# Kernel optimization log

Measured on AMD Instinct MI355X. Metric: run time of the kernel, lower is better.

Reference implementation:

```python
import jax, jax.numpy as jnp
import numpy as np

N, E, C = 50000, 10000, 500
NNZ = 400000
IN_DIM, EDGE_DIM, NODE_DIM, COMP_DIM = 128, 128, 128, 128


def _glorot(key, shape):
    fan = shape[0] + shape[1]
    return jax.random.normal(key, shape, jnp.float32) * (2.0 / fan) ** 0.5


def _seg_mean(vals, idx, num):
    # mean aggregation over segments (scatter-add + count normalize)
    s = jax.ops.segment_sum(vals, idx, num_segments=num)
    cnt = jax.ops.segment_sum(jnp.ones((idx.shape[0], 1), vals.dtype), idx, num_segments=num)
    return s / jnp.maximum(cnt, 1.0)


def _prelu(v, a):
    return jnp.where(v >= 0, v, a * v)


def _conv(x, ni, ei, ec_e, ec_c, nc_n, nc_c, n_nodes, n_edges, n_comps,
          Wne, Wen, Wec, Wnc, a):
    # node -> hyperedge message passing
    e = _seg_mean((x @ Wne)[ni], ei, n_edges)            # [E, edge_dim]
    e_act = _prelu(e, a)
    # hyperedge -> node
    n = _seg_mean((e_act @ Wen)[ei], ni, n_nodes)        # [N, node_dim]
    # edge -> component and node -> component
    c = _seg_mean((e_act @ Wec)[ec_e], ec_c, n_comps) + \
        _seg_mean((x @ Wnc)[nc_n], nc_c, n_comps)        # [C, comp_dim]
    return n, e, c


def setup_inputs() -> dict:
    key = jax.random.key(0)
    ks = jax.random.split(key, 16)
    x = jax.random.normal(ks[0], (N, IN_DIM), jnp.float32)
    hyperedge_index = jnp.stack([
        jax.random.randint(ks[1], (NNZ,), 0, N),
        jax.random.randint(ks[2], (NNZ,), 0, E),
    ])
    hyperedge_component_index = jnp.stack([
        jnp.arange(E), jax.random.randint(ks[3], (E,), 0, C)])
    node_component_index = jnp.stack([
        jnp.arange(N), jax.random.randint(ks[4], (N,), 0, C)])
    return dict(
        x=x,
        hyperedge_index=hyperedge_index,
        hyperedge_component_index=hyperedge_component_index,
        node_component_index=node_component_index,
        num_nodes=N, num_edges=E, num_components=C,
        W_ne0=_glorot(ks[5], (IN_DIM, EDGE_DIM)),
        W_en0=_glorot(ks[6], (EDGE_DIM, NODE_DIM)),
        W_ec0=_glorot(ks[7], (EDGE_DIM, COMP_DIM)),
        W_nc0=_glorot(ks[8], (IN_DIM, COMP_DIM)),
        W_ne1=_glorot(ks[9], (NODE_DIM, EDGE_DIM)),
        W_en1=_glorot(ks[10], (EDGE_DIM, NODE_DIM)),
        W_ec1=_glorot(ks[11], (EDGE_DIM, COMP_DIM)),
        W_nc1=_glorot(ks[12], (NODE_DIM, COMP_DIM)),
        prelu_a=jnp.array(0.25, jnp.float32),
    )


def reference(x, hyperedge_index, hyperedge_component_index, node_component_index,
              num_nodes, num_edges, num_components,
              W_ne0, W_en0, W_ec0, W_nc0, W_ne1, W_en1, W_ec1, W_nc1, prelu_a):
    ni, ei = hyperedge_index[0], hyperedge_index[1]
    ec_e, ec_c = hyperedge_component_index[0], hyperedge_component_index[1]
    nc_n, nc_c = node_component_index[0], node_component_index[1]
    layers = [(W_ne0, W_en0, W_ec0, W_nc0), (W_ne1, W_en1, W_ec1, W_nc1)]
    e_out = c_out = None
    for Wne, Wen, Wec, Wnc in layers:
        n_out, e_out, c_out = _conv(x, ni, ei, ec_e, ec_c, nc_n, nc_c,
                                    num_nodes, num_edges, num_components,
                                    Wne, Wen, Wec, Wnc, prelu_a)
        x = _prelu(n_out, prelu_a)  # HyperEncoder applies act between/after layers
    return (x, e_out, c_out)
```

## Files before the change

### kernel.cpp

```cpp
#include <hip/hip_runtime.h>
#include <stdint.h>

typedef unsigned int u32;
typedef _Float16 f16;
typedef f16 half8 __attribute__((ext_vector_type(8)));
typedef float f32x4 __attribute__((ext_vector_type(4)));
#define TS 4096
#define KB2 256
#define CH 2048

__device__ __forceinline__ float bflo(u32 u) { return __uint_as_float(u << 16); }
__device__ __forceinline__ float bfhi(u32 u) { return __uint_as_float(u & 0xffff0000u); }
__device__ __forceinline__ u32 f2bf(float x) {
    u32 u = __float_as_uint(x);
    return (u + 0x7fffu + ((u >> 16) & 1u)) >> 16;
}
__device__ __forceinline__ u32 pack2(float a, float b) { return f2bf(a) | (f2bf(b) << 16); }

__device__ __forceinline__ int bstart2(int b, int total) {
    return (int)(((unsigned long long)b * (u32)total + KB2 - 1) / KB2);
}

__device__ __forceinline__ int blk_exscan(int v, int& total) {
    __shared__ int ws[5];
    int t = threadIdx.x, lane = t & 63, w = t >> 6;
    int inc = v;
    for (int d = 1; d < 64; d <<= 1) { int u = __shfl_up(inc, d, 64); if (lane >= d) inc += u; }
    __syncthreads();
    if (lane == 63) ws[w] = inc;
    __syncthreads();
    if (t == 0) { int acc = 0; for (int i = 0; i < 4; ++i) { int x = ws[i]; ws[i] = acc; acc += x; } ws[4] = acc; }
    __syncthreads();
    total = ws[4];
    return ws[w] + (inc - v);
}

#define ACC8(v) do { \
    a[0] += bflo((v).x); a[1] += bfhi((v).x); a[2] += bflo((v).y); a[3] += bfhi((v).y); \
    a[4] += bflo((v).z); a[5] += bfhi((v).z); a[6] += bflo((v).w); a[7] += bfhi((v).w); } while (0)

__device__ __forceinline__ void seg_mean8(const u32* __restrict__ in,
                                          const int* __restrict__ items,
                                          const int* __restrict__ off,
                                          int nseg, int nrows, int seg, float a[8]) {
    int lane = threadIdx.x & 63;
    int rs = lane >> 4;
    int cc = lane & 15;
#pragma unroll
    for (int i = 0; i < 8; ++i) a[i] = 0.f;
    int s0 = 0, s1 = 0;
    if (seg < nseg) { s0 = off[seg]; s1 = off[seg + 1]; }
    const uint4* rows = (const uint4*)in;
    int base = s0;
    for (; base + 16 <= s1; base += 16) {
        u32 r0 = (u32)items[base + rs];
        u32 r1 = (u32)items[base + 4 + rs];
        u32 r2 = (u32)items[base + 8 + rs];
        u32 r3 = (u32)items[base + 12 + rs];
        r0 = (r0 < (u32)nrows) ? r0 : 0u;
        r1 = (r1 < (u32)nrows) ? r1 : 0u;
        r2 = (r2 < (u32)nrows) ? r2 : 0u;
        r3 = (r3 < (u32)nrows) ? r3 : 0u;
        uint4 v0 = rows[(size_t)r0 * 16 + cc];
        uint4 v1 = rows[(size_t)r1 * 16 + cc];
        uint4 v2 = rows[(size_t)r2 * 16 + cc];
        uint4 v3 = rows[(size_t)r3 * 16 + cc];
        ACC8(v0); ACC8(v1); ACC8(v2); ACC8(v3);
    }
    for (; base + 8 <= s1; base += 8) {
        u32 r0 = (u32)items[base + rs];
        u32 r1 = (u32)items[base + 4 + rs];
        r0 = (r0 < (u32)nrows) ? r0 : 0u;
        r1 = (r1 < (u32)nrows) ? r1 : 0u;
        uint4 v0 = rows[(size_t)r0 * 16 + cc];
        uint4 v1 = rows[(size_t)r1 * 16 + cc];
        ACC8(v0); ACC8(v1);
    }
    int idx = base + rs;
    if (idx < s1) {
        u32 r = (u32)items[idx]; r = (r < (u32)nrows) ? r : 0u;
        uint4 v = rows[(size_t)r * 16 + cc];
        ACC8(v);
    }
    idx += 4;
    if (idx < s1) {
        u32 r = (u32)items[idx]; r = (r < (u32)nrows) ? r : 0u;
        uint4 v = rows[(size_t)r * 16 + cc];
        ACC8(v);
    }
#pragma unroll
    for (int i = 0; i < 8; ++i) {
        a[i] += __shfl_xor(a[i], 16, 64);
        a[i] += __shfl_xor(a[i], 32, 64);
    }
    float inv = 1.f / fmaxf((float)(s1 - s0), 1.f);
#pragma unroll
    for (int i = 0; i < 8; ++i) a[i] *= inv;
}

__device__ __forceinline__ void agg4_body(const u32* __restrict__ in,
                                          const int* __restrict__ items,
                                          const int* __restrict__ off,
                                          float* __restrict__ out_f32,
                                          u32* __restrict__ out_bf,
                                          int nseg, int nrows, int do_prelu,
                                          const float* __restrict__ alpha_p, int seg,
                                          int nt) {
    if (seg >= nseg) return;
    int lane = threadIdx.x & 63;
    int rs = lane >> 4;
    int cc = lane & 15;
    float a[8];
    seg_mean8(in, items, off, nseg, nrows, seg, a);
    if (do_prelu) {
        float al = *alpha_p;
#pragma unroll
        for (int i = 0; i < 8; ++i) a[i] = (a[i] >= 0.f) ? a[i] : al * a[i];
    }
    if (rs == 0) {
        if (out_f32) {
            float* o = out_f32 + ((size_t)seg << 7) + cc * 8;
            f32x4 v0 = {a[0], a[1], a[2], a[3]};
            f32x4 v1 = {a[4], a[5], a[6], a[7]};
            if (nt) {
                __builtin_nontemporal_store(v0, (f32x4*)o);
                __builtin_nontemporal_store(v1, (f32x4*)(o + 4));
            } else {
                *(f32x4*)o = v0;
                *(f32x4*)(o + 4) = v1;
            }
        }
        if (out_bf) {
            uint4 pk;
            pk.x = pack2(a[0], a[1]); pk.y = pack2(a[2], a[3]);
            pk.z = pack2(a[4], a[5]); pk.w = pack2(a[6], a[7]);
            *(uint4*)(out_bf + ((size_t)seg << 6) + cc * 4) = pk;
        }
    }
}

__device__ __forceinline__ void aggh_body(const u32* __restrict__ in,
                                          const int* __restrict__ items,
                                          const int* __restrict__ off,
                                          f16* __restrict__ outh,
                                          int nseg, int nrows, int seg) {
    if (seg >= nseg) return;
    float a[8];
    seg_mean8(in, items, off, nseg, nrows, seg, a);
    int lane = threadIdx.x & 63, rs = lane >> 4, cc = lane & 15;
    if (rs == 0) {
        union { f16 h[8]; uint4 v; } u;
#pragma unroll
        for (int i = 0; i < 8; ++i) u.h[i] = (f16)a[i];
        *(uint4*)(outh + ((size_t)seg << 7) + cc * 8) = u.v;
    }
}

__device__ __forceinline__ void gemm1_body(const float* __restrict__ A,
                                           const f16* __restrict__ WL,
                                           float* __restrict__ out, int M,
                                           int rb, int accum, int nt) {
    int t = threadIdx.x, lane = t & 63, wv = t >> 6;
    int r0 = (wv >> 1) << 4, ctb = (wv & 1) << 2;
    int frow = lane & 15, fk = (lane >> 4) << 3;
    int rl0 = r0 + ((lane >> 4) << 2);
    int ar = rb + r0 + frow;
    f32x4 acc[4];
#pragma unroll
    for (int j = 0; j < 4; ++j) {
        int c = ((ctb + j) << 4) + frow;
#pragma unroll
        for (int rg = 0; rg < 4; ++rg) {
            int row = rb + rl0 + rg;
            acc[j][rg] = (accum && row < M) ? out[((size_t)row << 7) + c] : 0.f;
        }
    }
#pragma unroll
    for (int ks = 0; ks < 4; ++ks) {
        int kb = ks * 32 + fk;
        half8 af;
        if (ar < M) {
            float4 a0 = *(const float4*)(A + ((size_t)ar << 7) + kb);
            float4 a1 = *(const float4*)(A + ((size_t)ar << 7) + kb + 4);
            af[0] = (f16)a0.x; af[1] = (f16)a0.y; af[2] = (f16)a0.z; af[3] = (f16)a0.w;
            af[4] = (f16)a1.x; af[5] = (f16)a1.y; af[6] = (f16)a1.z; af[7] = (f16)a1.w;
        } else {
#pragma unroll
            for (int j = 0; j < 8; ++j) af[j] = (f16)0.f;
        }
#pragma unroll
        for (int j = 0; j < 4; ++j) {
            int c = ((ctb + j) << 4) + frow;
            half8 bf = *(const half8*)(WL + ((size_t)c << 7) + kb);
            acc[j] = __builtin_amdgcn_mfma_f32_16x16x32_f16(af, bf, acc[j], 0, 0, 0);
        }
    }
#pragma unroll
    for (int j = 0; j < 4; ++j) {
        int c = ((ctb + j) << 4) + frow;
#pragma unroll
        for (int rg = 0; rg < 4; ++rg) {
            int row = rb + rl0 + rg;
            if (row < M) {
                if (nt) __builtin_nontemporal_store(acc[j][rg], out + ((size_t)row << 7) + c);
                else out[((size_t)row << 7) + c] = acc[j][rg];
            }
        }
    }
}

__global__ __launch_bounds__(256) void k_front(
        const int* __restrict__ ni, const int* __restrict__ ei,
        const int* __restrict__ nc_c, const int* __restrict__ ec_c,
        int* __restrict__ bcntE, int* __restrict__ bcntN,
        int* __restrict__ cnt_cn, int* __restrict__ cnt_ce,
        int nnz, int n, int e, int nbh,
        int* __restrict__ ticket,
        int* __restrict__ basesE, int* __restrict__ basesN,
        int* __restrict__ bcur_e, int* __restrict__ bcur_n,
        int* __restrict__ off_cn, int* __restrict__ off_ce,
        int* __restrict__ cur_cn, int* __restrict__ cur_ce, int c,
        const float* __restrict__ W0, const float* __restrict__ W1,
        const float* __restrict__ W2, const float* __restrict__ W3,
        const float* __restrict__ W4, const float* __restrict__ W5,
        f16* __restrict__ wt6) {
    int t = threadIdx.x;
    int b = blockIdx.x;
    if (b >= nbh) {
        int gid = (b - nbh) * 256 + t;
        if (gid >= 8 * 2048) return;
        int m = gid >> 11;
        int rem = gid & 2047;
        int cq = rem >> 4;
        int s = rem & 15;
        const float* W = (m == 0) ? W0 : (m == 1) ? W1 : (m == 2) ? W2 :
                         (m == 3) ? W3 : (m == 4) ? W4 : (m == 5) ? W5 :
                         (m == 6) ? W4 : W5;
        int khi = (m < 6) ? (((s & 7) ^ (cq & 7)) | (s & 8)) : s;
        int k0 = khi << 3;
        union { f16 h[8]; uint4 v; } u;
#pragma unroll
        for (int j = 0; j < 8; ++j) u.h[j] = (f16)W[((k0 + j) << 7) + cq];
        *(uint4*)(wt6 + ((size_t)m << 14) + (cq << 7) + (s << 3)) = u.v;
        return;
    }
    __shared__ int hE[KB2], hN[KB2];
    __shared__ int lastflag;
    hE[t] = 0; hN[t] = 0;
    __syncthreads();
    int base = b * CH;
    int lim = base + CH; if (lim > nnz) lim = nnz;
    for (int i = base + t; i < lim; i += 256) {
        u32 v = (u32)ni[i], eg = (u32)ei[i];
        if (v >= (u32)n) v = 0;
        if (eg >= (u32)e) eg = 0;
        atomicAdd(&hE[(int)(((unsigned long long)eg * KB2) / (u32)e)], 1);
        atomicAdd(&hN[(int)(((unsigned long long)v  * KB2) / (u32)n)], 1);
    }
    __syncthreads();
    if (hE[t]) atomicAdd(&bcntE[t], hE[t]);
    if (hN[t]) atomicAdd(&bcntN[t], hN[t]);
    int gid = b * 256 + t, stride = nbh * 256;
    for (int j = gid; j < n + e; j += stride) {
        if (j < n) atomicAdd(&cnt_cn[nc_c[j]], 1);
        else       atomicAdd(&cnt_ce[ec_c[j - n]], 1);
    }
    __syncthreads();
    if (t == 0) {
        __threadfence();
        lastflag = (atomicAdd(ticket, 1) == nbh - 1);
    }
    __syncthreads();
    if (!lastflag) return;
    __threadfence();
    int tot;
    int v = bcntE[t];
    int ex = blk_exscan(v, tot);
    basesE[t] = ex; bcur_e[t] = ex;
    if (t == 0) basesE[KB2] = tot;
    v = bcntN[t];
    ex = blk_exscan(v, tot);
    basesN[t] = ex; bcur_n[t] = ex;
    if (t == 0) basesN[KB2] = tot;
    int i0 = 2 * t, i1 = 2 * t + 1;
    int v0 = (i0 < c) ? cnt_cn[i0] : 0;
    int v1 = (i1 < c) ? cnt_cn[i1] : 0;
    ex = blk_exscan(v0 + v1, tot);
    if (i0 < c) { off_cn[i0] = ex;      cur_cn[i0] = ex; }
    if (i1 < c) { off_cn[i1] = ex + v0; cur_cn[i1] = ex + v0; }
    if (t == 0) off_cn[c] = tot;
    v0 = (i0 < c) ? cnt_ce[i0] : 0;
    v1 = (i1 < c) ? cnt_ce[i1] : 0;
    ex = blk_exscan(v0 + v1, tot);
    if (i0 < c) { off_ce[i0] = ex;      cur_ce[i0] = ex; }
    if (i1 < c) { off_ce[i1] = ex + v0; cur_ce[i1] = ex + v0; }
    if (t == 0) off_ce[c] = tot;
}

__global__ __launch_bounds__(256) void k_part_a(
        const int* __restrict__ ni, const int* __restrict__ ei,
        int* __restrict__ bcur_e, int* __restrict__ bcur_n,
        u32* __restrict__ stg_e, u32* __restrict__ stg_n,
        const int* __restrict__ nc_n, const int* __restrict__ nc_c,
        const int* __restrict__ ec_e, const int* __restrict__ ec_c,
        int* __restrict__ cur_cn, int* __restrict__ cur_ce,
        int* __restrict__ csr_cn, int* __restrict__ csr_ce,
        const float2* __restrict__ xin, u32* __restrict__ xout, int npairs,
        int nnz, int n, int e, int nbh) {
    __shared__ u32 pk[CH];
    __shared__ unsigned short bb[CH];
    __shared__ int hist[KB2];
    __shared__ int gb[KB2];
    int t = threadIdx.x;
    int bx = blockIdx.x;
    if (bx >= 2 * nbh) {
        int j = (bx - 2 * nbh) * 256 + t;
        if (j < npairs) { float2 v = xin[j]; xout[j] = pack2(v.x, v.y); }
        return;
    }
    int side = bx >= nbh;
    int pb = side ? bx - nbh : bx;
    int base = pb * CH;
    int cnt  = nnz - base; if (cnt > CH) cnt = CH;
    for (int i = t; i < KB2; i += 256) hist[i] = 0;
    __syncthreads();
    u32 total = side ? (u32)n : (u32)e;
    for (int i = t; i < cnt; i += 256) {
        int v = ni[base + i], eg = ei[base + i];
        u32 key = side ? (u32)v : (u32)eg;
        u32 pay = side ? (u32)eg : (u32)v;
        if (key >= total) key = 0;
        u32 b = (u32)(((unsigned long long)key * KB2) / total);
        pk[i] = side ? (pay | (key << 14)) : (pay | (key << 16));
        bb[i] = (unsigned short)b;
        atomicAdd(&hist[b], 1);
    }
    __syncthreads();
    int* cursor = side ? bcur_n : bcur_e;
    u32* stg    = side ? stg_n  : stg_e;
    if (t < KB2) {
        int h = hist[t];
        gb[t] = h ? atomicAdd(&cursor[t], h) : 0;
        hist[t] = 0;
    }
    __syncthreads();
    for (int i = t; i < cnt; i += 256) {
        int b = bb[i];
        int r = atomicAdd(&hist[b], 1);
        stg[gb[b] + r] = pk[i];
    }
    int gid = pb * 256 + t;
    int stride = nbh * 256;
    if (side == 0) {
        for (int j = gid; j < e; j += stride) { int c = ec_c[j]; csr_ce[atomicAdd(&cur_ce[c], 1)] = ec_e[j]; }
    } else {
        for (int j = gid; j < n; j += stride) { int c = nc_c[j]; csr_cn[atomicAdd(&cur_cn[c], 1)] = nc_n[j]; }
    }
}

__global__ __launch_bounds__(256) void k_part_b2(
        const u32* __restrict__ stg_e, const u32* __restrict__ stg_n,
        const int* __restrict__ basesE, const int* __restrict__ basesN,
        int* __restrict__ off_e, int* __restrict__ off_n,
        int* __restrict__ csr_e, int* __restrict__ csr_n, int e, int n) {
    __shared__ int lcnt[256];
    int b = blockIdx.x, t = threadIdx.x;
    const u32* stg; const int* bases; int* off; int* csr; int total; int shift; u32 mask;
    if (b < KB2) { stg = stg_e; bases = basesE; off = off_e; csr = csr_e; total = e; shift = 16; mask = 0xFFFFu; }
    else { b -= KB2; stg = stg_n; bases = basesN; off = off_n; csr = csr_n; total = n; shift = 14; mask = 0x3FFFu; }
    int lo = bstart2(b, total), hi = bstart2(b + 1, total);
    int nid = hi - lo;
    int sbase = bases[b], send = bases[b + 1];
    lcnt[t] = 0;
    __syncthreads();
    for (int i = sbase + t; i < send; i += 256) {
        int key = (int)(stg[i] >> shift);
        atomicAdd(&lcnt[key - lo], 1);
    }
    __syncthreads();
    int cval = (t < nid) ? lcnt[t] : 0;
    int tot;
    int ex = blk_exscan(cval, tot);
    int cursor = sbase + ex;
    if (t < nid) { off[lo + t] = cursor; lcnt[t] = cursor; }
    if (t == 0 && hi == total) off[total] = send;
    __syncthreads();
    for (int i = sbase + t; i < send; i += 256) {
        u32 s = stg[i];
        int key = (int)(s >> shift);
        int pay = (int)(s & mask);
        int p = atomicAdd(&lcnt[key - lo], 1);
        csr[p] = pay;
    }
}

__global__ void k_cvt(const float2* __restrict__ in, u32* __restrict__ out, int npairs) {
    int j = blockIdx.x * blockDim.x + threadIdx.x;
    if (j < npairs) { float2 v = in[j]; out[j] = pack2(v.x, v.y); }
}

__global__ void k_hist_fb(const int* __restrict__ ni, const int* __restrict__ ei,
                          const int* __restrict__ nc_c, const int* __restrict__ ec_c,
                          int* __restrict__ deg_e, int* __restrict__ deg_n,
                          int* __restrict__ cnt_cn, int* __restrict__ cnt_ce,
                          int nnz, int n, int e) {
    int j = blockIdx.x * blockDim.x + threadIdx.x;
    if (j < nnz) {
        atomicAdd(&deg_e[ei[j]], 1);
        atomicAdd(&deg_n[ni[j]], 1);
    }
    if (j < n) atomicAdd(&cnt_cn[nc_c[j]], 1);
    if (j < e) atomicAdd(&cnt_ce[ec_c[j]], 1);
}

__device__ __forceinline__ void scan_sel(int b, int t0, int t01, int t012,
        const int* c0, int* o0, int* u0, int n0,
        const int* c1, int* o1, int* u1, int n1,
        const int* c2, int* o2, int* u2, int n2,
        const int* c3, int* o3, int* u3, int n3,
        const int*& cnt, int*& off, int*& cur, int& n, int& tile) {
    if (b < t0)        { cnt = c0; off = o0; cur = u0; n = n0; tile = b; }
    else if (b < t01)  { cnt = c1; off = o1; cur = u1; n = n1; tile = b - t0; }
    else if (b < t012) { cnt = c2; off = o2; cur = u2; n = n2; tile = b - t01; }
    else               { cnt = c3; off = o3; cur = u3; n = n3; tile = b - t012; }
}

__global__ void k_scan_p1(const int* c0, int n0, const int* c1, int n1,
                          const int* c2, int n2, const int* c3, int n3,
                          int t0, int t01, int t012, int* __restrict__ tilesum) {
    __shared__ int ws[4];
    int b = blockIdx.x;
    const int* cnt; int* off; int* cur; int n; int tile;
    scan_sel(b, t0, t01, t012, c0, nullptr, nullptr, n0, c1, nullptr, nullptr, n1,
             c2, nullptr, nullptr, n2, c3, nullptr, nullptr, n3, cnt, off, cur, n, tile);
    int base = tile * TS + threadIdx.x * 16;
    int s = 0;
#pragma unroll
    for (int i = 0; i < 16; ++i) { int idx = base + i; if (idx < n) s += cnt[idx]; }
    for (int d = 32; d; d >>= 1) s += __shfl_xor(s, d, 64);
    int lane = threadIdx.x & 63, w = threadIdx.x >> 6;
    if (lane == 0) ws[w] = s;
    __syncthreads();
    if (threadIdx.x == 0) tilesum[b] = ws[0] + ws[1] + ws[2] + ws[3];
}

__global__ void k_scan_p2(const int* __restrict__ tilesum, int* __restrict__ tilebase,
                          int t0, int t01, int t012, int t0123,
                          int* o0, int n0, int* o1, int n1, int* o2, int n2, int* o3, int n3) {
    if (threadIdx.x != 0 || blockIdx.x != 0) return;
    int carry = 0;
    for (int b = 0;    b < t0;    ++b) { tilebase[b] = carry; carry += tilesum[b]; } o0[n0] = carry;
    carry = 0;
    for (int b = t0;   b < t01;   ++b) { tilebase[b] = carry; carry += tilesum[b]; } o1[n1] = carry;
    carry = 0;
    for (int b = t01;  b < t012;  ++b) { tilebase[b] = carry; carry += tilesum[b]; } o2[n2] = carry;
    carry = 0;
    for (int b = t012; b < t0123; ++b) { tilebase[b] = carry; carry += tilesum[b]; } o3[n3] = carry;
}

__global__ void k_scan_p3(const int* c0, int* o0, int* u0, int n0,
                          const int* c1, int* o1, int* u1, int n1,
                          const int* c2, int* o2, int* u2, int n2,
                          const int* c3, int* o3, int* u3, int n3,
                          int t0, int t01, int t012, const int* __restrict__ tilebase) {
    __shared__ int wsum[4];
    int b = blockIdx.x;
    const int* cnt; int* off; int* cur; int n; int tile;
    scan_sel(b, t0, t01, t012, c0, o0, u0, n0, c1, o1, u1, n1,
             c2, o2, u2, n2, c3, o3, u3, n3, cnt, off, cur, n, tile);
    int lane = threadIdx.x & 63, w = threadIdx.x >> 6;
    int base = tile * TS + threadIdx.x * 16;
    int vals[16];
    int s = 0;
#pragma unroll
    for (int i = 0; i < 16; ++i) { int idx = base + i; int v = (idx < n) ? cnt[idx] : 0; vals[i] = v; s += v; }
    int inc = s;
    for (int d = 1; d < 64; d <<= 1) { int u = __shfl_up(inc, d, 64); if (lane >= d) inc += u; }
    if (lane == 63) wsum[w] = inc;
    __syncthreads();
    if (threadIdx.x == 0) {
        int acc = tilebase[b];
        for (int i = 0; i < 4; ++i) { int t = wsum[i]; wsum[i] = acc; acc += t; }
    }
    __syncthreads();
    int ex = wsum[w] + (inc - s);
#pragma unroll
    for (int i = 0; i < 16; ++i) {
        int idx = base + i;
        if (idx < n) { off[idx] = ex; cur[idx] = ex; }
        ex += vals[i];
    }
}

__global__ void k_scatter(const int* __restrict__ ni, const int* __restrict__ ei,
                          const int* __restrict__ nc_n, const int* __restrict__ nc_c,
                          const int* __restrict__ ec_e, const int* __restrict__ ec_c,
                          int* __restrict__ cur_e, int* __restrict__ cur_n,
                          int* __restrict__ cur_cn, int* __restrict__ cur_ce,
                          int* __restrict__ csr_e, int* __restrict__ csr_n,
                          int* __restrict__ csr_cn, int* __restrict__ csr_ce,
                          int nnz, int n, int e) {
    int j = blockIdx.x * blockDim.x + threadIdx.x;
    if (j < nnz) {
        int v = ni[j], eg = ei[j];
        csr_e[atomicAdd(&cur_e[eg], 1)] = v;
        csr_n[atomicAdd(&cur_n[v], 1)] = eg;
    }
    if (j < n) { int c = nc_c[j]; csr_cn[atomicAdd(&cur_cn[c], 1)] = nc_n[j]; }
    if (j < e) { int c = ec_c[j]; csr_ce[atomicAdd(&cur_ce[c], 1)] = ec_e[j]; }
}

__global__ __launch_bounds__(256) void k_agg4(
        const u32* __restrict__ in, const int* __restrict__ items,
        const int* __restrict__ off, float* __restrict__ out_f32,
        u32* __restrict__ out_bf,
        int nseg, int nrows, int do_prelu, const float* __restrict__ alpha_p) {
    int seg = blockIdx.x * (blockDim.x >> 6) + (threadIdx.x >> 6);
    agg4_body(in, items, off, out_f32, out_bf, nseg, nrows, do_prelu, alpha_p, seg, 0);
}

__global__ __launch_bounds__(256) void k_agg4h(
        const u32* __restrict__ in, const int* __restrict__ items,
        const int* __restrict__ off, f16* __restrict__ outh,
        int nseg, int nrows) {
    int seg = blockIdx.x * (blockDim.x >> 6) + (threadIdx.x >> 6);
    aggh_body(in, items, off, outh, nseg, nrows, seg);
}

__global__ __launch_bounds__(256) void k_agg_final(
        const u32* __restrict__ ybf, const int* __restrict__ csr_n, const int* __restrict__ off_n,
        float* __restrict__ out_x, int n, int e,
        const u32* __restrict__ eactbf, const int* __restrict__ csr_ce, const int* __restrict__ off_ce,
        float* __restrict__ ca_e,
        const float* __restrict__ ca_n, const f16* __restrict__ WncL,
        float* __restrict__ out_c,
        int c, int nblkN, int ncb, const float* __restrict__ alpha_p) {
    int b = blockIdx.x;
    int wv = threadIdx.x >> 6;
    if (b < nblkN) {
        agg4_body(ybf, csr_n, off_n, out_x, nullptr, n, e, 1, alpha_p, b * 4 + wv, 1);
    } else if (b < nblkN + ncb) {
        agg4_body(eactbf, csr_ce, off_ce, ca_e, nullptr, c, e, 0, nullptr, (b - nblkN) * 4 + wv, 0);
    } else {
        gemm1_body(ca_n, WncL, out_c, c, (b - nblkN - ncb) * 32, 0, 0);
    }
}

__global__ __launch_bounds__(256) void k_gemm1(
        const float* __restrict__ A, const f16* __restrict__ WL,
        float* __restrict__ out, int M) {
    gemm1_body(A, WL, out, M, blockIdx.x * 32, 1, 1);
}

__global__ __launch_bounds__(256) void k_mlp_mfma(
        const f16* __restrict__ Ah,
        const f16* __restrict__ W1t, const f16* __restrict__ W2t,
        float* __restrict__ out_raw, u32* __restrict__ out_actbf,
        u32* __restrict__ out_ybf, int M, const float* __restrict__ alpha_p,
        int nmlp,
        const u32* __restrict__ cn_in, const int* __restrict__ cn_items,
        const int* __restrict__ cn_off, float* __restrict__ cn_out,
        int cn_nseg, int cn_nrows) {
    __shared__ f16 As[32 * 128];
    __shared__ f16 Wt[128 * 128];
    int t = threadIdx.x;
    if (blockIdx.x >= nmlp) {
        if (cn_out == nullptr) return;
        int seg = (blockIdx.x - nmlp) * 4 + (t >> 6);
        agg4_body(cn_in, cn_items, cn_off, cn_out, nullptr, cn_nseg, cn_nrows, 0,
                  alpha_p, seg, 0);
        return;
    }
    int rb = blockIdx.x * 32;
    float al = *alpha_p;
    {
        const uint4* src = (const uint4*)W1t;
        uint4* dst = (uint4*)Wt;
        for (int i = t; i < 2048; i += 256) dst[i] = src[i];
    }
    {
        const uint4* Ag = (const uint4*)Ah;
        for (int i = t; i < 512; i += 256) {
            int r = i >> 4, s = i & 15;
            int row = rb + r;
            uint4 v = make_uint4(0u, 0u, 0u, 0u);
            if (row < M) v = Ag[(size_t)row * 16 + s];
            *(uint4*)((char*)As + (r << 8) + ((s << 4) ^ ((r & 7) << 4))) = v;
        }
    }
    __syncthreads();

    int lane = t & 63, wv = t >> 6;
    int r0  = (wv >> 1) << 4;
    int ctb = (wv & 1) << 2;
    int frow = lane & 15;
    int fk = (lane >> 4) << 3;
    int rl0 = r0 + ((lane >> 4) << 2);
    int ar = r0 + frow;
    int asw = (ar & 7) << 4;

    f32x4 acc[4] = {{0.f,0.f,0.f,0.f},{0.f,0.f,0.f,0.f},{0.f,0.f,0.f,0.f},{0.f,0.f,0.f,0.f}};
#pragma unroll
    for (int ks = 0; ks < 4; ++ks) {
        int kb2 = (ks * 32 + fk) << 1;
        half8 a = *(const half8*)((const char*)As + (ar << 8) + (kb2 ^ asw));
#pragma unroll
        for (int j = 0; j < 4; ++j) {
            int c = ((ctb + j) << 4) + frow;
            half8 b = *(const half8*)((const char*)Wt + (c << 8) + (kb2 ^ ((c & 7) << 4)));
            acc[j] = __builtin_amdgcn_mfma_f32_16x16x32_f16(a, b, acc[j], 0, 0, 0);
        }
    }
    __syncthreads();
    {
        const uint4* src = (const uint4*)W2t;
        uint4* dst = (uint4*)Wt;
        for (int i = t; i < 2048; i += 256) dst[i] = src[i];
    }
#pragma unroll
    for (int j = 0; j < 4; ++j) {
        int c = ((ctb + j) << 4) + frow;
#pragma unroll
        for (int rg = 0; rg < 4; ++rg) {
            int rl = rl0 + rg;
            int row = rb + rl;
            float ev = acc[j][rg];
            if (out_raw != nullptr && row < M)
                __builtin_nontemporal_store(ev, out_raw + ((size_t)row << 7) + c);
            float av = (ev >= 0.f) ? ev : al * ev;
            float po = __shfl_xor(av, 1, 64);
            if (out_actbf != nullptr && (frow & 1) == 0 && row < M)
                out_actbf[((size_t)row << 6) + (c >> 1)] = pack2(av, po);
            *(f16*)((char*)As + (rl << 8) + (((c << 1)) ^ ((rl & 7) << 4))) = (f16)av;
        }
    }
    __syncthreads();
    f32x4 acc2[4] = {{0.f,0.f,0.f,0.f},{0.f,0.f,0.f,0.f},{0.f,0.f,0.f,0.f},{0.f,0.f,0.f,0.f}};
#pragma unroll
    for (int ks = 0; ks < 4; ++ks) {
        int kb2 = (ks * 32 + fk) << 1;
        half8 a = *(const half8*)((const char*)As + (ar << 8) + (kb2 ^ asw));
#pragma unroll
        for (int j = 0; j < 4; ++j) {
            int c = ((ctb + j) << 4) + frow;
            half8 b = *(const half8*)((const char*)Wt + (c << 8) + (kb2 ^ ((c & 7) << 4)));
            acc2[j] = __builtin_amdgcn_mfma_f32_16x16x32_f16(a, b, acc2[j], 0, 0, 0);
        }
    }
#pragma unroll
    for (int j = 0; j < 4; ++j) {
        int c = ((ctb + j) << 4) + frow;
#pragma unroll
        for (int rg = 0; rg < 4; ++rg) {
            int rl = rl0 + rg;
            int row = rb + rl;
            float yv = acc2[j][rg];
            float po = __shfl_xor(yv, 1, 64);
            if ((frow & 1) == 0 && row < M)
                out_ybf[((size_t)row << 6) + (c >> 1)] = pack2(yv, po);
        }
    }
}

extern "C" void kernel_launch(void* const* d_in, const int* in_sizes, int n_in,
                              void* d_out, int out_size, void* d_ws, size_t ws_size,
                              hipStream_t stream) {
    const int N   = in_sizes[0] / 128;
    const int NNZ = in_sizes[1] / 2;
    const int E   = in_sizes[2] / 2;
    const int C   = 500;

    const float* x0 = (const float*)d_in[0];
    const int* ni   = (const int*)d_in[1];
    const int* ei   = ni + NNZ;
    const int* ec_e = (const int*)d_in[2];
    const int* ec_c = ec_e + E;
    const int* nc_n = (const int*)d_in[3];
    const int* nc_c = nc_n + N;
    const float* Wne0 = (const float*)d_in[7];
    const float* Wen0 = (const float*)d_in[8];
    const float* Wne1 = (const float*)d_in[11];
    const float* Wen1 = (const float*)d_in[12];
    const float* Wec1 = (const float*)d_in[13];
    const float* Wnc1 = (const float*)d_in[14];
    const float* alpha = (const float*)d_in[15];

    float* out_x = (float*)d_out;
    float* out_e = out_x + (size_t)N * 128;
    float* out_c = out_e + (size_t)E * 128;

    char* w = (char*)d_ws;
    auto alloc = [&](size_t bytes) { char* p = w; w += (bytes + 255) & ~(size_t)255; return p; };
    int* zgrp   = (int*)alloc((size_t)(2 * KB2 + 2 * C + 1) * 4);
    int* bcntE  = zgrp;
    int* bcntN  = zgrp + KB2;
    int* cnt_cn = zgrp + 2 * KB2;
    int* cnt_ce = zgrp + 2 * KB2 + C;
    int* ticket = zgrp + 2 * KB2 + 2 * C;
    int* off_e  = (int*)alloc((size_t)(E + 1) * 4);
    int* off_n  = (int*)alloc((size_t)(N + 1) * 4);
    int* off_cn = (int*)alloc((size_t)(C + 1) * 4);
    int* off_ce = (int*)alloc((size_t)(C + 1) * 4);
    int* cur_cn = (int*)alloc((size_t)C * 4);
    int* cur_ce = (int*)alloc((size_t)C * 4);
    int* csr_e  = (int*)alloc((size_t)NNZ * 4);
    int* csr_n  = (int*)alloc((size_t)NNZ * 4);
    int* csr_cn = (int*)alloc((size_t)N * 4);
    int* csr_ce = (int*)alloc((size_t)E * 4);
    int* basesE = (int*)alloc((size_t)(KB2 + 1) * 4);
    int* basesN = (int*)alloc((size_t)(KB2 + 1) * 4);
    int* bcur_e = (int*)alloc(KB2 * 4);
    int* bcur_n = (int*)alloc(KB2 * 4);
    u32* stg_e  = (u32*)alloc((size_t)NNZ * 4);
    u32* stg_n  = (u32*)alloc((size_t)NNZ * 4);
    u32* xbf    = (u32*)alloc((size_t)N * 64 * 4);
    u32* x1bf   = (u32*)alloc((size_t)N * 64 * 4);
    u32* ybf    = (u32*)alloc((size_t)E * 64 * 4);
    u32* eactbf = (u32*)alloc((size_t)E * 64 * 4);
    f16* xah    = (f16*)alloc((size_t)E * 128 * 2);
    float* ca_e = (float*)alloc((size_t)C * 128 * 4);
    float* ca_n = (float*)alloc((size_t)C * 128 * 4);
    f16* wt6    = (f16*)alloc((size_t)8 * 16384 * 2);
    int* deg_e    = (int*)alloc((size_t)E * 4);
    int* deg_n    = (int*)alloc((size_t)N * 4);
    int* cur_e    = (int*)alloc((size_t)E * 4);
    int* cur_n    = (int*)alloc((size_t)N * 4);
    int* tilesum  = (int*)alloc(64 * 4);
    int* tilebase = (int*)alloc(64 * 4);

    const int th = 256;
    const int npairs = N * 64;
    const int nbh = (NNZ + CH - 1) / CH;
    const int nkc = (npairs + th - 1) / th;

    bool binned = (E <= 16384) && (N <= 65536) && (E >= KB2) && (N >= KB2) &&
                  ((N + KB2 - 1) / KB2 <= 256) && (C <= 512);
    const int nbh_eff = binned ? nbh : 0;

    hipMemsetAsync(zgrp, 0, (size_t)(2 * KB2 + 2 * C + 1) * 4, stream);
    k_front<<<nbh_eff + 64, 256, 0, stream>>>(
        ni, ei, nc_c, ec_c,
        bcntE, bcntN, cnt_cn, cnt_ce, NNZ, N, E, nbh_eff,
        ticket, basesE, basesN, bcur_e, bcur_n,
        off_cn, off_ce, cur_cn, cur_ce, C,
        Wne0, Wen0, Wne1, Wen1, Wec1, Wnc1, wt6);

    if (binned) {
        k_part_a<<<2 * nbh + nkc, 256, 0, stream>>>(
            ni, ei, bcur_e, bcur_n, stg_e, stg_n,
            nc_n, nc_c, ec_e, ec_c,
            cur_cn, cur_ce, csr_cn, csr_ce,
            (const float2*)x0, xbf, npairs, NNZ, N, E, nbh);
        k_part_b2<<<2 * KB2, 256, 0, stream>>>(stg_e, stg_n, basesE, basesN,
                                               off_e, off_n, csr_e, csr_n, E, N);
    } else {
        hipMemsetAsync(deg_e, 0, (size_t)E * 4, stream);
        hipMemsetAsync(deg_n, 0, (size_t)N * 4, stream);
        k_cvt<<<(npairs + th - 1) / th, th, 0, stream>>>((const float2*)x0, xbf, npairs);
        k_hist_fb<<<(NNZ > N + E ? NNZ : N + E) / th + 1, th, 0, stream>>>(
            ni, ei, nc_c, ec_c, deg_e, deg_n, cnt_cn, cnt_ce, NNZ, N, E);
        const int t0 = (E + TS - 1) / TS, t1 = (N + TS - 1) / TS;
        const int t2 = (C + TS - 1) / TS, t3 = (C + TS - 1) / TS;
        const int t01 = t0 + t1, t012 = t01 + t2, t0123 = t012 + t3;
        k_scan_p1<<<t0123, 256, 0, stream>>>(deg_e, E, deg_n, N, cnt_cn, C, cnt_ce, C,
                                             t0, t01, t012, tilesum);
        k_scan_p2<<<1, 64, 0, stream>>>(tilesum, tilebase, t0, t01, t012, t0123,
                                        off_e, E, off_n, N, off_cn, C, off_ce, C);
        k_scan_p3<<<t0123, 256, 0, stream>>>(deg_e, off_e, cur_e, E,
                                             deg_n, off_n, cur_n, N,
                                             cnt_cn, off_cn, cur_cn, C,
                                             cnt_ce, off_ce, cur_ce, C,
                                             t0, t01, t012, tilebase);
        k_scatter<<<(NNZ + th - 1) / th, th, 0, stream>>>(ni, ei, nc_n, nc_c, ec_e, ec_c,
                                                          cur_e, cur_n, cur_cn, cur_ce,
                                                          csr_e, csr_n, csr_cn, csr_ce, NNZ, N, E);
    }

    const int gmlp = (E + 31) / 32;
    const int ncb  = (C + 3) / 4;
    const int gc   = (C + 31) / 32;
    k_agg4h<<<(E + 3) / 4, 256, 0, stream>>>(xbf, csr_e, off_e, xah, E, N);
    k_mlp_mfma<<<gmlp, 256, 0, stream>>>(xah, wt6, wt6 + 16384, nullptr, nullptr, ybf,
                                         E, alpha, gmlp,
                                         nullptr, nullptr, nullptr, nullptr, 0, 0);
    k_agg4<<<(N + 3) / 4, 256, 0, stream>>>(ybf, csr_n, off_n, nullptr, x1bf, N, E, 1, alpha);
    k_agg4h<<<(E + 3) / 4, 256, 0, stream>>>(x1bf, csr_e, off_e, xah, E, N);
    k_mlp_mfma<<<gmlp + ncb, 256, 0, stream>>>(xah, wt6 + 2 * 16384, wt6 + 3 * 16384,
                                               out_e, eactbf, ybf, E, alpha, gmlp,
                                               x1bf, csr_cn, off_cn, ca_n, C, N);
    {
        const int nblkN = (N + 3) / 4;
        k_agg_final<<<nblkN + ncb + gc, 256, 0, stream>>>(
            ybf, csr_n, off_n, out_x, N, E,
            eactbf, csr_ce, off_ce, ca_e,
            ca_n, wt6 + 7 * 16384, out_c,
            C, nblkN, ncb, alpha);
    }
    k_gemm1<<<gc, 256, 0, stream>>>(ca_e, wt6 + 6 * 16384, out_c, C);
}
```

Before: 256.7 us.

## Vectorize CSR index loads in segment mean and merge binning passes

The segment-mean gather now loads neighbor indices as 16-byte and 8-byte vectors, and adds a 32-item unrolled loop so more row loads are in flight per lane. It also changes which item each lane accumulates, which is fine because summation order is free. The partition kernel now bins each nnz chunk for both the edge and node sides in a single block. This halves the grid and reads the ni/ei arrays once instead of twice. The tradeoffs are doubled shared memory per block and lower block-level parallelism in the partition step.

```diff
diff --git a/kernel.cpp b/kernel.cpp
--- a/kernel.cpp
+++ b/kernel.cpp
@@ -5,6 +5,8 @@
 typedef _Float16 f16;
 typedef f16 half8 __attribute__((ext_vector_type(8)));
 typedef float f32x4 __attribute__((ext_vector_type(4)));
+typedef uint4 uint4u __attribute__((aligned(4)));
+typedef uint2 uint2u __attribute__((aligned(4)));
 #define TS 4096
 #define KB2 256
 #define CH 2048
@@ -52,15 +54,31 @@
     if (seg < nseg) { s0 = off[seg]; s1 = off[seg + 1]; }
     const uint4* rows = (const uint4*)in;
     int base = s0;
+    for (; base + 32 <= s1; base += 32) {
+        uint4 i0 = *(const uint4u*)&items[base + rs * 4];
+        uint4 i1 = *(const uint4u*)&items[base + 16 + rs * 4];
+        u32 r0 = i0.x, r1 = i0.y, r2 = i0.z, r3 = i0.w;
+        u32 r4 = i1.x, r5 = i1.y, r6 = i1.z, r7 = i1.w;
+        r0 = (r0 < (u32)nrows) ? r0 : 0u;  r1 = (r1 < (u32)nrows) ? r1 : 0u;
+        r2 = (r2 < (u32)nrows) ? r2 : 0u;  r3 = (r3 < (u32)nrows) ? r3 : 0u;
+        r4 = (r4 < (u32)nrows) ? r4 : 0u;  r5 = (r5 < (u32)nrows) ? r5 : 0u;
+        r6 = (r6 < (u32)nrows) ? r6 : 0u;  r7 = (r7 < (u32)nrows) ? r7 : 0u;
+        uint4 v0 = rows[(size_t)r0 * 16 + cc];
+        uint4 v1 = rows[(size_t)r1 * 16 + cc];
+        uint4 v2 = rows[(size_t)r2 * 16 + cc];
+        uint4 v3 = rows[(size_t)r3 * 16 + cc];
+        uint4 v4 = rows[(size_t)r4 * 16 + cc];
+        uint4 v5 = rows[(size_t)r5 * 16 + cc];
+        uint4 v6 = rows[(size_t)r6 * 16 + cc];
+        uint4 v7 = rows[(size_t)r7 * 16 + cc];
+        ACC8(v0); ACC8(v1); ACC8(v2); ACC8(v3);
+        ACC8(v4); ACC8(v5); ACC8(v6); ACC8(v7);
+    }
     for (; base + 16 <= s1; base += 16) {
-        u32 r0 = (u32)items[base + rs];
-        u32 r1 = (u32)items[base + 4 + rs];
-        u32 r2 = (u32)items[base + 8 + rs];
-        u32 r3 = (u32)items[base + 12 + rs];
-        r0 = (r0 < (u32)nrows) ? r0 : 0u;
-        r1 = (r1 < (u32)nrows) ? r1 : 0u;
-        r2 = (r2 < (u32)nrows) ? r2 : 0u;
-        r3 = (r3 < (u32)nrows) ? r3 : 0u;
+        uint4 i0 = *(const uint4u*)&items[base + rs * 4];
+        u32 r0 = i0.x, r1 = i0.y, r2 = i0.z, r3 = i0.w;
+        r0 = (r0 < (u32)nrows) ? r0 : 0u;  r1 = (r1 < (u32)nrows) ? r1 : 0u;
+        r2 = (r2 < (u32)nrows) ? r2 : 0u;  r3 = (r3 < (u32)nrows) ? r3 : 0u;
         uint4 v0 = rows[(size_t)r0 * 16 + cc];
         uint4 v1 = rows[(size_t)r1 * 16 + cc];
         uint4 v2 = rows[(size_t)r2 * 16 + cc];
@@ -68,8 +86,8 @@
         ACC8(v0); ACC8(v1); ACC8(v2); ACC8(v3);
     }
     for (; base + 8 <= s1; base += 8) {
-        u32 r0 = (u32)items[base + rs];
-        u32 r1 = (u32)items[base + 4 + rs];
+        uint2 i0 = *(const uint2u*)&items[base + rs * 2];
+        u32 r0 = i0.x, r1 = i0.y;
         r0 = (r0 < (u32)nrows) ? r0 : 0u;
         r1 = (r1 < (u32)nrows) ? r1 : 0u;
         uint4 v0 = rows[(size_t)r0 * 16 + cc];
@@ -307,55 +325,58 @@
         int* __restrict__ csr_cn, int* __restrict__ csr_ce,
         const float2* __restrict__ xin, u32* __restrict__ xout, int npairs,
         int nnz, int n, int e, int nbh) {
-    __shared__ u32 pk[CH];
-    __shared__ unsigned short bb[CH];
-    __shared__ int hist[KB2];
-    __shared__ int gb[KB2];
     int t = threadIdx.x;
     int bx = blockIdx.x;
-    if (bx >= 2 * nbh) {
-        int j = (bx - 2 * nbh) * 256 + t;
+    if (bx >= nbh) {
+        int j = (bx - nbh) * 256 + t;
         if (j < npairs) { float2 v = xin[j]; xout[j] = pack2(v.x, v.y); }
         return;
     }
-    int side = bx >= nbh;
-    int pb = side ? bx - nbh : bx;
-    int base = pb * CH;
+    __shared__ u32 pkE[CH];
+    __shared__ u32 pkN[CH];
+    __shared__ unsigned short bbE[CH];
+    __shared__ unsigned short bbN[CH];
+    __shared__ int histE[KB2], histN[KB2];
+    __shared__ int gbE[KB2], gbN[KB2];
+    int base = bx * CH;
     int cnt  = nnz - base; if (cnt > CH) cnt = CH;
-    for (int i = t; i < KB2; i += 256) hist[i] = 0;
-    __syncthreads();
-    u32 total = side ? (u32)n : (u32)e;
+    for (int i = t; i < KB2; i += 256) { histE[i] = 0; histN[i] = 0; }
+    __syncthreads();
     for (int i = t; i < cnt; i += 256) {
-        int v = ni[base + i], eg = ei[base + i];
-        u32 key = side ? (u32)v : (u32)eg;
-        u32 pay = side ? (u32)eg : (u32)v;
-        if (key >= total) key = 0;
-        u32 b = (u32)(((unsigned long long)key * KB2) / total);
-        pk[i] = side ? (pay | (key << 14)) : (pay | (key << 16));
-        bb[i] = (unsigned short)b;
-        atomicAdd(&hist[b], 1);
-    }
-    __syncthreads();
-    int* cursor = side ? bcur_n : bcur_e;
-    u32* stg    = side ? stg_n  : stg_e;
+        u32 v = (u32)ni[base + i], eg = (u32)ei[base + i];
+        if (v >= (u32)n) v = 0;
+        if (eg >= (u32)e) eg = 0;
+        u32 bE = (u32)(((unsigned long long)eg * KB2) / (u32)e);
+        u32 bN = (u32)(((unsigned long long)v  * KB2) / (u32)n);
+        pkE[i] = v | (eg << 16);
+        pkN[i] = eg | (v << 14);
+        bbE[i] = (unsigned short)bE;
+        bbN[i] = (unsigned short)bN;
+        atomicAdd(&histE[bE], 1);
+        atomicAdd(&histN[bN], 1);
+    }
+    __syncthreads();
     if (t < KB2) {
-        int h = hist[t];
-        gb[t] = h ? atomicAdd(&cursor[t], h) : 0;
-        hist[t] = 0;
+        int h = histE[t];
+        gbE[t] = h ? atomicAdd(&bcur_e[t], h) : 0;
+        histE[t] = 0;
+        h = histN[t];
+        gbN[t] = h ? atomicAdd(&bcur_n[t], h) : 0;
+        histN[t] = 0;
     }
     __syncthreads();
     for (int i = t; i < cnt; i += 256) {
-        int b = bb[i];
-        int r = atomicAdd(&hist[b], 1);
-        stg[gb[b] + r] = pk[i];
-    }
-    int gid = pb * 256 + t;
+        int b = bbE[i];
+        int r = atomicAdd(&histE[b], 1);
+        stg_e[gbE[b] + r] = pkE[i];
+        b = bbN[i];
+        r = atomicAdd(&histN[b], 1);
+        stg_n[gbN[b] + r] = pkN[i];
+    }
+    int gid = bx * 256 + t;
     int stride = nbh * 256;
-    if (side == 0) {
-        for (int j = gid; j < e; j += stride) { int c = ec_c[j]; csr_ce[atomicAdd(&cur_ce[c], 1)] = ec_e[j]; }
-    } else {
-        for (int j = gid; j < n; j += stride) { int c = nc_c[j]; csr_cn[atomicAdd(&cur_cn[c], 1)] = nc_n[j]; }
-    }
+    for (int j = gid; j < e; j += stride) { int c = ec_c[j]; csr_ce[atomicAdd(&cur_ce[c], 1)] = ec_e[j]; }
+    for (int j = gid; j < n; j += stride) { int c = nc_c[j]; csr_cn[atomicAdd(&cur_cn[c], 1)] = nc_n[j]; }
 }
 
 __global__ __launch_bounds__(256) void k_part_b2(
@@ -746,7 +767,7 @@
         Wne0, Wen0, Wne1, Wen1, Wec1, Wnc1, wt6);
 
     if (binned) {
-        k_part_a<<<2 * nbh + nkc, 256, 0, stream>>>(
+        k_part_a<<<nbh + nkc, 256, 0, stream>>>(
             ni, ei, bcur_e, bcur_n, stg_e, stg_n,
             nc_n, nc_c, ec_e, ec_c,
             cur_cn, cur_ce, csr_cn, csr_ce,
```

After: 269.8 us. +5.1%, slower.
